# Performance work log

Measured on AMD Instinct MI355X. Metric: run time of the kernel, lower is better.

Reference implementation:

```python
import jax, jax.numpy as jnp
import numpy as np
import math

B, N, CS, CZ, H, C, P, PV, NB = 1, 512, 384, 128, 12, 16, 4, 8, 64


def quat_to_rot(q):
    q = q / jnp.clip(jnp.linalg.norm(q, axis=-1, keepdims=True), 1e-8)
    w, x, y, z = q[..., 0], q[..., 1], q[..., 2], q[..., 3]
    return jnp.stack([
        w*w + x*x - y*y - z*z, 2*(x*y - w*z), 2*(x*z + w*y),
        2*(x*y + w*z), w*w - x*x + y*y - z*z, 2*(y*z - w*x),
        2*(x*z - w*y), 2*(y*z + w*x), w*w - x*x - y*y + z*z,
    ], axis=-1).reshape(q.shape[:-1] + (3, 3))


def setup_inputs() -> dict:
    key = jax.random.key(0)
    ks = jax.random.split(key, 28)
    def n(k, shape, sc=1.0):
        return jax.random.normal(k, shape, jnp.float32) * sc
    s = n(ks[0], (B, N, CS))
    z = n(ks[1], (B, N, N, CZ))
    translations = n(ks[2], (B, N, 3)) * 4.0  # spread distances over 0-32A bins
    rotations = quat_to_rot(n(ks[3], (B, N, 4)))  # valid SO(3) frames
    mask = jnp.ones((B, N), dtype=bool)
    inv = lambda fan: 1.0 / math.sqrt(fan)
    return {
        's': s, 'z': z, 'translations': translations, 'rotations': rotations, 'mask': mask,
        'Wq': n(ks[4], (CS, H*C), inv(CS)), 'bq': n(ks[5], (H*C,), 0.01),
        'Wk': n(ks[6], (CS, H*C), inv(CS)), 'bk': n(ks[7], (H*C,), 0.01),
        'Wv': n(ks[8], (CS, H*C), inv(CS)), 'bv': n(ks[9], (H*C,), 0.01),
        'Wqp': n(ks[10], (CS, H*P*3), inv(CS)), 'bqp': n(ks[11], (H*P*3,), 0.01),
        'Wkp': n(ks[12], (CS, H*P*3), inv(CS)), 'bkp': n(ks[13], (H*P*3,), 0.01),
        'Wvp': n(ks[14], (CS, H*PV*3), inv(CS)), 'bvp': n(ks[15], (H*PV*3,), 0.01),
        'Wb': n(ks[16], (CZ, H), inv(CZ)), 'bb': n(ks[17], (H,), 0.01),
        'dist_emb': n(ks[18], (NB, H), 0.02),
        'scale_logits': n(ks[19], (3, H), 0.1),
        'head_weights': jnp.abs(n(ks[20], (H,))) * 0.2 + 0.8,
        'Wout': n(ks[21], (H*(C + PV*4 + CZ), CS), inv(H*(C + PV*4 + CZ))),
        'bout': n(ks[22], (CS,), 0.01),
    }


def reference(s, z, translations, rotations, mask, Wq, bq, Wk, bk, Wv, bv,
              Wqp, bqp, Wkp, bkp, Wvp, bvp, Wb, bb, dist_emb, scale_logits,
              head_weights, Wout, bout):
    b, n, _ = s.shape
    q = (s @ Wq + bq).reshape(b, n, H, C)
    k = (s @ Wk + bk).reshape(b, n, H, C)
    v = (s @ Wv + bv).reshape(b, n, H, C)
    q_pts = (s @ Wqp + bqp).reshape(b, n, H, P, 3)
    k_pts = (s @ Wkp + bkp).reshape(b, n, H, P, 3)
    v_pts = (s @ Wvp + bvp).reshape(b, n, H, PV, 3)
    t = translations[:, :, None, None, :]
    q_g = jnp.einsum('bnij,bnhpj->bnhpi', rotations, q_pts) + t
    k_g = jnp.einsum('bnij,bnhpj->bnhpi', rotations, k_pts) + t
    v_g = jnp.einsum('bnij,bnhpj->bnhpi', rotations, v_pts) + t
    scalar_logits = jnp.einsum('bnhc,bmhc->bnmh', q, k) / math.sqrt(C)
    # squared point distances, summed over points p and coords i, via expansion
    q_sq = (q_g**2).sum((-1, -2))  # (b, n, h)
    k_sq = (k_g**2).sum((-1, -2))
    cross = jnp.einsum('bnhpi,bmhpi->bnmh', q_g, k_g)
    point_dist = q_sq[:, :, None, :] + k_sq[:, None, :, :] - 2.0 * cross
    point_logits = -0.5 * point_dist * head_weights
    pair_bias = z @ Wb + bb  # (b, n, m, h)
    pair_dist = jnp.linalg.norm(
        translations[:, :, None, :] - translations[:, None, :, :], axis=-1)
    edges = jnp.linspace(0.0, 32.0, NB + 1)
    bins = jnp.clip(jnp.searchsorted(edges, pair_dist, side='left') - 1, 0, NB - 1)
    dist_bias = dist_emb[bins]
    local = (pair_dist <= 5.0).astype(s.dtype)
    medium = ((pair_dist > 5.0) & (pair_dist <= 15.0)).astype(s.dtype)
    scales = jnp.stack([local, medium, jnp.ones_like(pair_dist)], axis=-1)
    per_head = jax.nn.softmax(scale_logits, axis=0)  # (3, h)
    multiscale = jnp.einsum('bnms,sh->bnmh', scales, per_head)
    logits = scalar_logits + point_logits + pair_bias + dist_bias + multiscale
    m2d = mask[:, :, None] & mask[:, None, :]
    logits = jnp.where(m2d[..., None], logits, -10000.0)
    attn = jax.nn.softmax(logits.astype(jnp.float32), axis=2).astype(s.dtype)
    out_scalar = jnp.einsum('bnmh,bmhc->bnhc', attn, v)
    out_pts_g = jnp.einsum('bnmh,bmhpi->bnhpi', attn, v_g)
    out_pts_l = jnp.einsum('bnji,bnhpj->bnhpi', rotations, out_pts_g - t)  # R^T x
    out_norms = jnp.linalg.norm(out_pts_l, axis=-1)  # (b, n, h, pv)
    pair_feat = jnp.einsum('bnmh,bnmc->bnhc', attn, z)
    feats = jnp.concatenate(
        [out_scalar, out_pts_l.reshape(b, n, H, PV * 3), out_norms, pair_feat],
        axis=-1).reshape(b, n, -1)
    return feats @ Wout + bout
```

## Files before the change

### kernel.cpp

```cpp
#include <hip/hip_runtime.h>
#include <math.h>

#define N   512
#define CS  384
#define CZ  128
#define H   12
#define C   16
#define P   4
#define PV  8
#define NB  64
#define KSP 528
#define QKD 28
#define QPAD 68
#define APAD 516
#define ZPAD 132

#define OFF_Q    0
#define OFF_K    98304
#define OFF_V    196608
#define OFF_QP   294912
#define OFF_KP   368640
#define OFF_VP   442368
#define OFF_QG   589824
#define OFF_KG   663552
#define OFF_VG   737280
#define OFF_QSQ  884736
#define OFF_KSQ  890880
#define OFF_LOG  897024
#define OFF_FEAT 4042752

__global__ __launch_bounds__(256) void k_proj(
    const float* __restrict__ s,
    const float* __restrict__ Wq,  const float* __restrict__ bq,
    const float* __restrict__ Wk,  const float* __restrict__ bk,
    const float* __restrict__ Wv,  const float* __restrict__ bv,
    const float* __restrict__ Wqp, const float* __restrict__ bqp,
    const float* __restrict__ Wkp, const float* __restrict__ bkp,
    const float* __restrict__ Wvp, const float* __restrict__ bvp,
    float* __restrict__ ws)
{
    __shared__ float s_s[16*388];
    __shared__ float part[4*16*68];
    const int tid = threadIdx.x;
    const int n0  = blockIdx.y * 16;
    const int cq  = tid & 15;
    const int rg  = (tid >> 4) & 3;
    const int ks  = tid >> 6;
    const int gc  = blockIdx.x * 64 + cq * 4;
    for (int i = tid; i < 16*384; i += 256) {
        int r = i / 384, c = i - r*384;
        s_s[r*388 + c] = s[(n0 + r)*384 + c];
    }
    __syncthreads();
    const float* W; int width; int lc;
    if      (gc < 192) { W=Wq;  width=192; lc=gc;     }
    else if (gc < 384) { W=Wk;  width=192; lc=gc-192; }
    else if (gc < 576) { W=Wv;  width=192; lc=gc-384; }
    else if (gc < 720) { W=Wqp; width=144; lc=gc-576; }
    else if (gc < 864) { W=Wkp; width=144; lc=gc-720; }
    else               { W=Wvp; width=288; lc=gc-864; }
    float acc[4][4] = {{0.f}};
    const float* wp   = W + lc + (size_t)(ks*96)*width;
    const float* srow = s_s + (rg*4)*388 + ks*96;
    #pragma unroll 4
    for (int kk = 0; kk < 96; kk++) {
        float4 w4 = *(const float4*)(wp + (size_t)kk*width);
        #pragma unroll
        for (int r = 0; r < 4; r++) {
            float sv = srow[r*388 + kk];
            acc[r][0] += sv*w4.x; acc[r][1] += sv*w4.y;
            acc[r][2] += sv*w4.z; acc[r][3] += sv*w4.w;
        }
    }
    #pragma unroll
    for (int r = 0; r < 4; r++)
        *(float4*)(part + (ks*16 + rg*4 + r)*68 + cq*4) =
            make_float4(acc[r][0], acc[r][1], acc[r][2], acc[r][3]);
    __syncthreads();
    {
        const int row = tid >> 4;
        float4 sum = *(const float4*)(part + (0*16 + row)*68 + cq*4);
        #pragma unroll
        for (int k2 = 1; k2 < 4; k2++) {
            float4 p = *(const float4*)(part + (k2*16 + row)*68 + cq*4);
            sum.x += p.x; sum.y += p.y; sum.z += p.z; sum.w += p.w;
        }
        const float* b; float* dst; int w2, lc2;
        if      (gc < 192) { b=bq;  w2=192; lc2=gc;     dst=ws+OFF_Q;  }
        else if (gc < 384) { b=bk;  w2=192; lc2=gc-192; dst=ws+OFF_K;  }
        else if (gc < 576) { b=bv;  w2=192; lc2=gc-384; dst=ws+OFF_V;  }
        else if (gc < 720) { b=bqp; w2=144; lc2=gc-576; dst=ws+OFF_QP; }
        else if (gc < 864) { b=bkp; w2=144; lc2=gc-720; dst=ws+OFF_KP; }
        else               { b=bvp; w2=288; lc2=gc-864; dst=ws+OFF_VP; }
        float4 b4 = *(const float4*)(b + lc2);
        sum.x += b4.x; sum.y += b4.y; sum.z += b4.z; sum.w += b4.w;
        *(float4*)(dst + (size_t)(n0+row)*w2 + lc2) = sum;
    }
}

__global__ __launch_bounds__(192) void k_frames(
    const float* __restrict__ rot, const float* __restrict__ trans,
    float* __restrict__ ws)
{
    int n = blockIdx.x, tid = threadIdx.x;
    __shared__ float R[9], T[3], qg_s[144], kg_s[144];
    if (tid < 9) R[tid] = rot[n*9 + tid];
    if (tid < 3) T[tid] = trans[n*3 + tid];
    __syncthreads();
    if (tid < 48) {
        const float* lp = ws + OFF_QP + n*144 + tid*3;
        float l0=lp[0], l1=lp[1], l2=lp[2];
        float* gp = ws + OFF_QG + n*144 + tid*3;
        for (int i=0;i<3;i++){ float g = R[i*3+0]*l0 + R[i*3+1]*l1 + R[i*3+2]*l2 + T[i]; gp[i]=g; qg_s[tid*3+i]=g; }
    } else if (tid < 96) {
        int u = tid-48;
        const float* lp = ws + OFF_KP + n*144 + u*3;
        float l0=lp[0], l1=lp[1], l2=lp[2];
        float* gp = ws + OFF_KG + n*144 + u*3;
        for (int i=0;i<3;i++){ float g = R[i*3+0]*l0 + R[i*3+1]*l1 + R[i*3+2]*l2 + T[i]; gp[i]=g; kg_s[u*3+i]=g; }
    } else {
        int u = tid-96;
        const float* lp = ws + OFF_VP + n*288 + u*3;
        float l0=lp[0], l1=lp[1], l2=lp[2];
        float* gp = ws + OFF_VG + n*288 + u*3;
        for (int i=0;i<3;i++){ float g = R[i*3+0]*l0 + R[i*3+1]*l1 + R[i*3+2]*l2 + T[i]; gp[i]=g; }
    }
    __syncthreads();
    if (tid < 12) {
        float a=0;
        for (int d=0; d<12; d++){ float x=qg_s[tid*12+d]; a+=x*x; }
        ws[OFF_QSQ + n*12 + tid]=a;
    } else if (tid < 24) {
        int h = tid-12; float a=0;
        for (int d=0; d<12; d++){ float x=kg_s[h*12+d]; a+=x*x; }
        ws[OFF_KSQ + n*12 + h]=a;
    }
}

__global__ __launch_bounds__(256) void k_qkpt(
    const float* __restrict__ head_weights, float* __restrict__ ws)
{
    __shared__ float qs[QKD*QPAD], ks[QKD*QPAD], qa[64], kb[64];
    const int tid = threadIdx.x;
    const int m0 = blockIdx.x * 64, n0 = blockIdx.y * 64, h = blockIdx.z;
    const float hw = head_weights[h];
    for (int idx = tid; idx < 64*16; idx += 256) {
        int r = idx >> 4, c = idx & 15;
        qs[c*QPAD + r] = ws[OFF_Q + (n0+r)*192 + h*16 + c] * 0.25f;
        ks[c*QPAD + r] = ws[OFF_K + (m0+r)*192 + h*16 + c];
    }
    for (int idx = tid; idx < 64*12; idx += 256) {
        int r = idx / 12, c = idx % 12;
        qs[(16+c)*QPAD + r] = ws[OFF_QG + (n0+r)*144 + h*12 + c] * hw;
        ks[(16+c)*QPAD + r] = ws[OFF_KG + (m0+r)*144 + h*12 + c];
    }
    for (int idx = tid; idx < 64; idx += 256) {
        qa[idx] = -0.5f * hw * ws[OFF_QSQ + (n0+idx)*12 + h];
        kb[idx] = -0.5f * hw * ws[OFF_KSQ + (m0+idx)*12 + h];
    }
    __syncthreads();
    const int tx = tid & 15, ty = tid >> 4;
    float acc[4][4] = {{0.f}};
    #pragma unroll 4
    for (int d = 0; d < QKD; d++) {
        float4 a = *(const float4*)(qs + d*QPAD + ty*4);
        float4 b = *(const float4*)(ks + d*QPAD + tx*4);
        const float* ap = &a.x; const float* bp = &b.x;
        #pragma unroll
        for (int i=0;i<4;i++)
            #pragma unroll
            for (int j=0;j<4;j++) acc[i][j] += ap[i]*bp[j];
    }
    #pragma unroll
    for (int i=0;i<4;i++) {
        float ai = qa[ty*4+i];
        float4 r;
        r.x = acc[i][0] + ai + kb[tx*4+0];
        r.y = acc[i][1] + ai + kb[tx*4+1];
        r.z = acc[i][2] + ai + kb[tx*4+2];
        r.w = acc[i][3] + ai + kb[tx*4+3];
        *(float4*)(ws + OFF_LOG + ((size_t)(n0+ty*4+i)*H + h)*N + m0 + tx*4) = r;
    }
}

__global__ __launch_bounds__(256) void k_attn_all(
    const float* __restrict__ z, const float* __restrict__ trans,
    const float* __restrict__ rot,
    const float* __restrict__ Wb, const float* __restrict__ bb,
    const float* __restrict__ dist_emb, const float* __restrict__ scale_logits,
    float* __restrict__ ws)
{
    __shared__ float attn_s[H*APAD];
    __shared__ float zs[64*ZPAD];
    __shared__ float partial[4*64*13];
    __shared__ float Wb_s[CZ*12];
    __shared__ float og_s[288];
    __shared__ float sprob[36];
    float* part = zs;
    const int n = blockIdx.x, tid = threadIdx.x;
    const int lane = tid & 63, wave = tid >> 6;

    if (tid < 12) {
        float sa = scale_logits[tid], sb = scale_logits[12+tid], sc = scale_logits[24+tid];
        float mx = fmaxf(sa, fmaxf(sb, sc));
        float ea=__expf(sa-mx), eb=__expf(sb-mx), ec=__expf(sc-mx);
        float inv = 1.f/(ea+eb+ec);
        sprob[tid] = ea*inv; sprob[12+tid] = eb*inv; sprob[24+tid] = ec*inv;
    }
    for (int i = tid; i < 384; i += 256)
        *(float4*)(Wb_s + i*4) = *(const float4*)(Wb + i*4);

    const float4* asrc = (const float4*)(ws + OFF_LOG + (size_t)n*H*N);
    for (int i = tid; i < H*(N/4); i += 256) {
        int h = i >> 7, q = i & 127;
        *(float4*)(attn_s + h*APAD + q*4) = asrc[h*128 + q];
    }
    __syncthreads();

    {
        const float tnx = trans[n*3+0], tny = trans[n*3+1], tnz = trans[n*3+2];
        const int h0 = wave*3;
        const float bbv0 = bb[h0], bbv1 = bb[h0+1], bbv2 = bb[h0+2];
        const float spc0 = sprob[24+h0], spc1 = sprob[24+h0+1], spc2 = sprob[24+h0+2];
        const float spa0 = sprob[h0],    spa1 = sprob[h0+1],    spa2 = sprob[h0+2];
        const float spb0 = sprob[12+h0], spb1 = sprob[12+h0+1], spb2 = sprob[12+h0+2];
        const float4* zsrc4 = (const float4*)(z + (size_t)n*N*CZ);
        for (int chunk = 0; chunk < 8; chunk++) {
            #pragma unroll
            for (int pass = 0; pass < 8; pass++) {
                int idx = pass*256 + tid;
                float4 v = zsrc4[chunk*2048 + idx];
                *(float4*)(zs + (idx>>5)*ZPAD + (idx&31)*4) = v;
            }
            __syncthreads();
            {
                const float* zrow = zs + lane*ZPAD + wave*32;
                float a[12];
                #pragma unroll
                for (int h=0;h<12;h++) a[h]=0.f;
                #pragma unroll
                for (int c4=0;c4<8;c4++) {
                    float4 zq = *(const float4*)(zrow + c4*4);
                    const float* wr = Wb_s + (wave*32 + c4*4)*12;
                    const float* zp = &zq.x;
                    #pragma unroll
                    for (int j=0;j<4;j++) {
                        float4 w0 = *(const float4*)(wr + j*12);
                        float4 w1 = *(const float4*)(wr + j*12 + 4);
                        float4 w2 = *(const float4*)(wr + j*12 + 8);
                        float zj = zp[j];
                        a[0]+=zj*w0.x; a[1]+=zj*w0.y; a[2]+=zj*w0.z; a[3]+=zj*w0.w;
                        a[4]+=zj*w1.x; a[5]+=zj*w1.y; a[6]+=zj*w1.z; a[7]+=zj*w1.w;
                        a[8]+=zj*w2.x; a[9]+=zj*w2.y; a[10]+=zj*w2.z; a[11]+=zj*w2.w;
                    }
                }
                float* pdst = partial + (wave*64 + lane)*13;
                #pragma unroll
                for (int h=0;h<12;h++) pdst[h] = a[h];
            }
            __syncthreads();
            {
                const int m = chunk*64 + lane;
                float dx = tnx - trans[m*3+0];
                float dy = tny - trans[m*3+1];
                float dz = tnz - trans[m*3+2];
                float pdist = sqrtf(dx*dx+dy*dy+dz*dz);
                int bin = (int)ceilf(2.f*pdist) - 1;
                bin = bin < 0 ? 0 : (bin > NB-1 ? NB-1 : bin);
                const int ssel = (pdist <= 5.f) ? 0 : (pdist <= 15.f ? 1 : -1);
                float v0 = partial[(0*64+lane)*13 + h0]   + partial[(1*64+lane)*13 + h0]
                         + partial[(2*64+lane)*13 + h0]   + partial[(3*64+lane)*13 + h0];
                float v1 = partial[(0*64+lane)*13 + h0+1] + partial[(1*64+lane)*13 + h0+1]
                         + partial[(2*64+lane)*13 + h0+1] + partial[(3*64+lane)*13 + h0+1];
                float v2 = partial[(0*64+lane)*13 + h0+2] + partial[(1*64+lane)*13 + h0+2]
                         + partial[(2*64+lane)*13 + h0+2] + partial[(3*64+lane)*13 + h0+2];
                v0 += bbv0 + dist_emb[bin*12 + h0]   + spc0;
                v1 += bbv1 + dist_emb[bin*12 + h0+1] + spc1;
                v2 += bbv2 + dist_emb[bin*12 + h0+2] + spc2;
                if (ssel == 0)      { v0 += spa0; v1 += spa1; v2 += spa2; }
                else if (ssel == 1) { v0 += spb0; v1 += spb1; v2 += spb2; }
                attn_s[(h0  )*APAD + m] += v0;
                attn_s[(h0+1)*APAD + m] += v1;
                attn_s[(h0+2)*APAD + m] += v2;
            }
            __syncthreads();
        }
    }

    for (int h = wave; h < H; h += 4) {
        float* row = attn_s + h*APAD;
        float v[8]; float mx = -1e30f;
        #pragma unroll
        for (int j=0;j<8;j++){ v[j]=row[lane + j*64]; mx = fmaxf(mx, v[j]); }
        #pragma unroll
        for (int off=32; off>0; off>>=1) mx = fmaxf(mx, __shfl_xor(mx, off, 64));
        float sum = 0.f;
        #pragma unroll
        for (int j=0;j<8;j++){ v[j]=__expf(v[j]-mx); sum += v[j]; }
        #pragma unroll
        for (int off=32; off>0; off>>=1) sum += __shfl_xor(sum, off, 64);
        float inv = 1.f/sum;
        #pragma unroll
        for (int j=0;j<8;j++) row[lane + j*64] = v[j]*inv;
    }
    __syncthreads();

    const int cq = tid & 15;
    const int ms = tid >> 4;
    for (int ch = 0; ch < 2; ch++) {
        const float* zb = z + (size_t)n*N*CZ + ch*64 + cq*4;
        float4 acc[12];
        #pragma unroll
        for (int h=0; h<12; h++) acc[h] = make_float4(0.f,0.f,0.f,0.f);
        const int r0 = ms*32;
        #pragma unroll 2
        for (int rq = 0; rq < 8; rq++) {
            const int r = r0 + rq*4;
            float4 z0 = *(const float4*)(zb + (size_t)(r+0)*CZ);
            float4 z1 = *(const float4*)(zb + (size_t)(r+1)*CZ);
            float4 z2 = *(const float4*)(zb + (size_t)(r+2)*CZ);
            float4 z3 = *(const float4*)(zb + (size_t)(r+3)*CZ);
            #pragma unroll
            for (int h=0; h<12; h++) {
                float4 a4 = *(const float4*)(attn_s + h*APAD + r);
                acc[h].x += a4.x*z0.x + a4.y*z1.x + a4.z*z2.x + a4.w*z3.x;
                acc[h].y += a4.x*z0.y + a4.y*z1.y + a4.z*z2.y + a4.w*z3.y;
                acc[h].z += a4.x*z0.z + a4.y*z1.z + a4.z*z2.z + a4.w*z3.z;
                acc[h].w += a4.x*z0.w + a4.y*z1.w + a4.z*z2.w + a4.w*z3.w;
            }
        }
        #pragma unroll
        for (int h=0; h<12; h++) {
            acc[h].x += __shfl_xor(acc[h].x, 16, 64); acc[h].y += __shfl_xor(acc[h].y, 16, 64);
            acc[h].z += __shfl_xor(acc[h].z, 16, 64); acc[h].w += __shfl_xor(acc[h].w, 16, 64);
            acc[h].x += __shfl_xor(acc[h].x, 32, 64); acc[h].y += __shfl_xor(acc[h].y, 32, 64);
            acc[h].z += __shfl_xor(acc[h].z, 32, 64); acc[h].w += __shfl_xor(acc[h].w, 32, 64);
        }
        if (lane < 16) {
            #pragma unroll
            for (int h=0; h<12; h++)
                *(float4*)(part + (wave*12 + h)*64 + lane*4) = acc[h];
        }
        __syncthreads();
        if (tid < 192) {
            const int h = tid >> 4, c4 = tid & 15;
            float4 s4 = *(const float4*)(part + (0*12 + h)*64 + c4*4);
            #pragma unroll
            for (int w=1; w<4; w++) {
                float4 p = *(const float4*)(part + (w*12 + h)*64 + c4*4);
                s4.x += p.x; s4.y += p.y; s4.z += p.z; s4.w += p.w;
            }
            *(float4*)(ws + OFF_FEAT + (size_t)n*2112 + h*176 + 48 + ch*64 + c4*4) = s4;
        }
        __syncthreads();
    }

    if (tid < 240) {
        const int col4 = (tid % 120) * 4;
        const int msA  = tid / 120;
        const float* aptr; int astride, ah;
        if (col4 < 192) { ah = col4 >> 4;        aptr = ws + OFF_V  + col4;       astride = 192; }
        else            { ah = (col4-192) / 24;  aptr = ws + OFF_VG + (col4-192); astride = 288; }
        const float4* arow = (const float4*)(attn_s + ah*APAD);
        float4 acc = {0.f,0.f,0.f,0.f};
        #pragma unroll 2
        for (int mq = msA*64; mq < msA*64 + 64; mq++) {
            float4 a4 = arow[mq];
            const float* vp = aptr + (size_t)mq*4*astride;
            float4 v0 = *(const float4*)(vp);
            float4 v1 = *(const float4*)(vp + astride);
            float4 v2 = *(const float4*)(vp + 2*astride);
            float4 v3 = *(const float4*)(vp + 3*astride);
            acc.x += a4.x*v0.x + a4.y*v1.x + a4.z*v2.x + a4.w*v3.x;
            acc.y += a4.x*v0.y + a4.y*v1.y + a4.z*v2.y + a4.w*v3.y;
            acc.z += a4.x*v0.z + a4.y*v1.z + a4.z*v2.z + a4.w*v3.z;
            acc.w += a4.x*v0.w + a4.y*v1.w + a4.z*v2.w + a4.w*v3.w;
        }
        *(float4*)(part + tid*4) = acc;
    }
    __syncthreads();
    if (tid < 120) {
        const int col4 = tid * 4;
        float4 a = *(const float4*)(part + tid*4);
        float4 b = *(const float4*)(part + (tid+120)*4);
        a.x += b.x; a.y += b.y; a.z += b.z; a.w += b.w;
        if (col4 < 192) {
            const int ah = col4 >> 4;
            *(float4*)(ws + OFF_FEAT + (size_t)n*2112 + ah*176 + (col4 & 15)) = a;
        } else {
            *(float4*)(og_s + (col4 - 192)) = a;
        }
    }
    __syncthreads();
    if (tid < 96) {
        const int h = tid >> 3, p = tid & 7;
        float g0 = og_s[h*24 + p*3 + 0] - trans[n*3+0];
        float g1 = og_s[h*24 + p*3 + 1] - trans[n*3+1];
        float g2 = og_s[h*24 + p*3 + 2] - trans[n*3+2];
        const float* R = rot + n*9;
        float* fdst = ws + OFF_FEAT + (size_t)n*2112 + h*176;
        float nsq = 0.f;
        #pragma unroll
        for (int i=0;i<3;i++){
            float l = R[0*3+i]*g0 + R[1*3+i]*g1 + R[2*3+i]*g2;
            fdst[16 + p*3 + i] = l;
            nsq += l*l;
        }
        fdst[40 + p] = sqrtf(nsq);
    }
}

__global__ __launch_bounds__(384) void k_bias(
    const float* __restrict__ bout, float* __restrict__ out)
{
    out[(size_t)blockIdx.x*CS + threadIdx.x] = bout[threadIdx.x];
}

__global__ __launch_bounds__(256) void k_out(
    const float* __restrict__ Wout, const float* __restrict__ ws,
    float* __restrict__ out)
{
    __shared__ float f_s[16*KSP];
    __shared__ float part[4*16*68];
    const int tid = threadIdx.x;
    const int n0  = blockIdx.y * 16;
    const int k0  = blockIdx.z * KSP;
    const int cq  = tid & 15;
    const int rg  = (tid >> 4) & 3;
    const int ks  = tid >> 6;
    const int col = blockIdx.x * 64 + cq * 4;
    for (int i = tid; i < 16*KSP; i += 256) {
        int r = i / KSP, c = i - r*KSP;
        f_s[i] = ws[OFF_FEAT + (size_t)(n0 + r)*2112 + k0 + c];
    }
    __syncthreads();
    float acc[4][4] = {{0.f}};
    const float* wp = Wout + (size_t)(k0 + ks*132)*CS + col;
    const float* f0 = f_s + (rg*4)*KSP + ks*132;
    #pragma unroll 4
    for (int kk = 0; kk < 132; kk++) {
        float4 w4 = *(const float4*)(wp + (size_t)kk*CS);
        #pragma unroll
        for (int r = 0; r < 4; r++) {
            float fv = f0[r*KSP + kk];
            acc[r][0] += fv*w4.x; acc[r][1] += fv*w4.y;
            acc[r][2] += fv*w4.z; acc[r][3] += fv*w4.w;
        }
    }
    #pragma unroll
    for (int r = 0; r < 4; r++)
        *(float4*)(part + (ks*16 + rg*4 + r)*68 + cq*4) =
            make_float4(acc[r][0], acc[r][1], acc[r][2], acc[r][3]);
    __syncthreads();
    {
        const int row = tid >> 4;
        float4 s = *(const float4*)(part + (0*16 + row)*68 + cq*4);
        #pragma unroll
        for (int k2 = 1; k2 < 4; k2++) {
            float4 p = *(const float4*)(part + (k2*16 + row)*68 + cq*4);
            s.x += p.x; s.y += p.y; s.z += p.z; s.w += p.w;
        }
        float* o = out + (size_t)(n0+row)*CS + col;
        atomicAdd(o+0, s.x); atomicAdd(o+1, s.y);
        atomicAdd(o+2, s.z); atomicAdd(o+3, s.w);
    }
}

extern "C" void kernel_launch(void* const* d_in, const int* in_sizes, int n_in,
                              void* d_out, int out_size, void* d_ws, size_t ws_size,
                              hipStream_t stream) {
    const float* s     = (const float*)d_in[0];
    const float* z     = (const float*)d_in[1];
    const float* trans = (const float*)d_in[2];
    const float* rot   = (const float*)d_in[3];
    const float* Wq  = (const float*)d_in[5];  const float* bq  = (const float*)d_in[6];
    const float* Wk  = (const float*)d_in[7];  const float* bk  = (const float*)d_in[8];
    const float* Wv  = (const float*)d_in[9];  const float* bv  = (const float*)d_in[10];
    const float* Wqp = (const float*)d_in[11]; const float* bqp = (const float*)d_in[12];
    const float* Wkp = (const float*)d_in[13]; const float* bkp = (const float*)d_in[14];
    const float* Wvp = (const float*)d_in[15]; const float* bvp = (const float*)d_in[16];
    const float* Wb  = (const float*)d_in[17]; const float* bb  = (const float*)d_in[18];
    const float* dist_emb     = (const float*)d_in[19];
    const float* scale_logits = (const float*)d_in[20];
    const float* head_weights = (const float*)d_in[21];
    const float* Wout = (const float*)d_in[22]; const float* bout = (const float*)d_in[23];
    float* out = (float*)d_out;
    float* ws  = (float*)d_ws;

    k_proj<<<dim3(18, 32), 256, 0, stream>>>(s, Wq,bq, Wk,bk, Wv,bv, Wqp,bqp, Wkp,bkp, Wvp,bvp, ws);
    k_frames<<<N, 192, 0, stream>>>(rot, trans, ws);
    k_qkpt<<<dim3(8, 8, 12), 256, 0, stream>>>(head_weights, ws);
    k_attn_all<<<N, 256, 0, stream>>>(z, trans, rot, Wb, bb, dist_emb, scale_logits, ws);
    k_bias<<<N, CS, 0, stream>>>(bout, out);
    k_out<<<dim3(6, 32, 4), 256, 0, stream>>>(Wout, ws, out);
}
```

Baseline: 364.9 us.

## Split fused attention kernel into z-bias, softmax, and role-split matmul kernels

Breaks the monolithic per-row attention kernel into three launches. A z-bias kernel spreads each row's pair-bias work over four blocks and adds it to the logits in global memory. A separate softmax kernel normalises the logits in place. The aggregation kernel then runs two blocks per row: one computes the attention-weighted z features, the other the scalar and point value aggregation plus the frame transform. This raises the number of blocks and cuts per-block LDS use to improve occupancy. In exchange, the logits make extra round trips through global memory and there are two more kernel launches.

```diff
diff --git a/kernel.cpp b/kernel.cpp
--- a/kernel.cpp
+++ b/kernel.cpp
@@ -13,7 +13,7 @@
 #define QKD 28
 #define QPAD 68
 #define APAD 516
-#define ZPAD 132
+#define ZP2 132
 
 #define OFF_Q    0
 #define OFF_K    98304
@@ -183,22 +183,18 @@
     }
 }
 
-__global__ __launch_bounds__(256) void k_attn_all(
+__global__ __launch_bounds__(256) void k_zbias2(
     const float* __restrict__ z, const float* __restrict__ trans,
-    const float* __restrict__ rot,
     const float* __restrict__ Wb, const float* __restrict__ bb,
     const float* __restrict__ dist_emb, const float* __restrict__ scale_logits,
     float* __restrict__ ws)
 {
-    __shared__ float attn_s[H*APAD];
-    __shared__ float zs[64*ZPAD];
+    __shared__ float zs[64*ZP2];
     __shared__ float partial[4*64*13];
     __shared__ float Wb_s[CZ*12];
-    __shared__ float og_s[288];
     __shared__ float sprob[36];
-    float* part = zs;
-    const int n = blockIdx.x, tid = threadIdx.x;
-    const int lane = tid & 63, wave = tid >> 6;
+    const int mb = blockIdx.x, n = blockIdx.y;
+    const int tid = threadIdx.x, lane = tid & 63, wave = tid >> 6;
 
     if (tid < 12) {
         float sa = scale_logits[tid], sb = scale_logits[12+tid], sc = scale_logits[24+tid];
@@ -209,6 +205,110 @@
     }
     for (int i = tid; i < 384; i += 256)
         *(float4*)(Wb_s + i*4) = *(const float4*)(Wb + i*4);
+    __syncthreads();
+
+    const float tnx = trans[n*3+0], tny = trans[n*3+1], tnz = trans[n*3+2];
+    const int h0 = wave*3;
+
+    for (int chunk = 0; chunk < 2; chunk++) {
+        const int m0 = mb*128 + chunk*64;
+        const float4* zsrc4 = (const float4*)(z + ((size_t)n*N + m0)*CZ);
+        #pragma unroll
+        for (int p = 0; p < 8; p++) {
+            int idx = p*256 + tid;
+            float4 v = zsrc4[idx];
+            *(float4*)(zs + (idx>>5)*ZP2 + (idx&31)*4) = v;
+        }
+        __syncthreads();
+        {
+            const float* zrow = zs + lane*ZP2 + wave*32;
+            float a[12];
+            #pragma unroll
+            for (int h=0;h<12;h++) a[h]=0.f;
+            #pragma unroll
+            for (int c4=0;c4<8;c4++) {
+                float4 zq = *(const float4*)(zrow + c4*4);
+                const float* wr = Wb_s + (wave*32 + c4*4)*12;
+                const float* zp = &zq.x;
+                #pragma unroll
+                for (int j=0;j<4;j++) {
+                    float4 w0 = *(const float4*)(wr + j*12);
+                    float4 w1 = *(const float4*)(wr + j*12 + 4);
+                    float4 w2 = *(const float4*)(wr + j*12 + 8);
+                    float zj = zp[j];
+                    a[0]+=zj*w0.x; a[1]+=zj*w0.y; a[2]+=zj*w0.z; a[3]+=zj*w0.w;
+                    a[4]+=zj*w1.x; a[5]+=zj*w1.y; a[6]+=zj*w1.z; a[7]+=zj*w1.w;
+                    a[8]+=zj*w2.x; a[9]+=zj*w2.y; a[10]+=zj*w2.z; a[11]+=zj*w2.w;
+                }
+            }
+            float* pdst = partial + (wave*64 + lane)*13;
+            #pragma unroll
+            for (int h=0;h<12;h++) pdst[h] = a[h];
+        }
+        __syncthreads();
+        {
+            const int m = m0 + lane;
+            float dx = tnx - trans[m*3+0];
+            float dy = tny - trans[m*3+1];
+            float dz = tnz - trans[m*3+2];
+            float pdist = sqrtf(dx*dx+dy*dy+dz*dz);
+            int bin = (int)ceilf(2.f*pdist) - 1;
+            bin = bin < 0 ? 0 : (bin > NB-1 ? NB-1 : bin);
+            const int ssel = (pdist <= 5.f) ? 0 : (pdist <= 15.f ? 1 : -1);
+            float v0 = partial[(0*64+lane)*13 + h0]   + partial[(1*64+lane)*13 + h0]
+                     + partial[(2*64+lane)*13 + h0]   + partial[(3*64+lane)*13 + h0];
+            float v1 = partial[(0*64+lane)*13 + h0+1] + partial[(1*64+lane)*13 + h0+1]
+                     + partial[(2*64+lane)*13 + h0+1] + partial[(3*64+lane)*13 + h0+1];
+            float v2 = partial[(0*64+lane)*13 + h0+2] + partial[(1*64+lane)*13 + h0+2]
+                     + partial[(2*64+lane)*13 + h0+2] + partial[(3*64+lane)*13 + h0+2];
+            v0 += bb[h0]   + dist_emb[bin*12 + h0]   + sprob[24+h0];
+            v1 += bb[h0+1] + dist_emb[bin*12 + h0+1] + sprob[24+h0+1];
+            v2 += bb[h0+2] + dist_emb[bin*12 + h0+2] + sprob[24+h0+2];
+            if (ssel == 0)      { v0 += sprob[h0];    v1 += sprob[h0+1];    v2 += sprob[h0+2]; }
+            else if (ssel == 1) { v0 += sprob[12+h0]; v1 += sprob[12+h0+1]; v2 += sprob[12+h0+2]; }
+            float* lp = ws + OFF_LOG + ((size_t)n*H + h0)*N + m;
+            lp[0]   += v0;
+            lp[N]   += v1;
+            lp[2*N] += v2;
+        }
+        __syncthreads();
+    }
+}
+
+__global__ __launch_bounds__(256) void k_sm(float* __restrict__ ws)
+{
+    const int n = blockIdx.x, tid = threadIdx.x;
+    const int lane = tid & 63, wave = tid >> 6;
+    for (int h = wave; h < H; h += 4) {
+        float* row = ws + OFF_LOG + ((size_t)n*H + h)*N;
+        float4 a = *(const float4*)(row + lane*8);
+        float4 b = *(const float4*)(row + lane*8 + 4);
+        float mx = fmaxf(fmaxf(fmaxf(a.x,a.y),fmaxf(a.z,a.w)),
+                         fmaxf(fmaxf(b.x,b.y),fmaxf(b.z,b.w)));
+        #pragma unroll
+        for (int off=32; off>0; off>>=1) mx = fmaxf(mx, __shfl_xor(mx, off, 64));
+        a.x=__expf(a.x-mx); a.y=__expf(a.y-mx); a.z=__expf(a.z-mx); a.w=__expf(a.w-mx);
+        b.x=__expf(b.x-mx); b.y=__expf(b.y-mx); b.z=__expf(b.z-mx); b.w=__expf(b.w-mx);
+        float sum = a.x+a.y+a.z+a.w+b.x+b.y+b.z+b.w;
+        #pragma unroll
+        for (int off=32; off>0; off>>=1) sum += __shfl_xor(sum, off, 64);
+        float inv = 1.f/sum;
+        a.x*=inv; a.y*=inv; a.z*=inv; a.w*=inv;
+        b.x*=inv; b.y*=inv; b.z*=inv; b.w*=inv;
+        *(float4*)(row + lane*8)     = a;
+        *(float4*)(row + lane*8 + 4) = b;
+    }
+}
+
+__global__ __launch_bounds__(256) void k_attnmm(
+    const float* __restrict__ z, const float* __restrict__ trans,
+    const float* __restrict__ rot, float* __restrict__ ws)
+{
+    __shared__ float attn_s[H*APAD];
+    __shared__ float part[4*12*64];
+    __shared__ float og_s[288];
+    const int n = blockIdx.x, role = blockIdx.y, tid = threadIdx.x;
+    const int lane = tid & 63, wave = tid >> 6;
 
     const float4* asrc = (const float4*)(ws + OFF_LOG + (size_t)n*H*N);
     for (int i = tid; i < H*(N/4); i += 256) {
@@ -217,196 +317,110 @@
     }
     __syncthreads();
 
-    {
-        const float tnx = trans[n*3+0], tny = trans[n*3+1], tnz = trans[n*3+2];
-        const int h0 = wave*3;
-        const float bbv0 = bb[h0], bbv1 = bb[h0+1], bbv2 = bb[h0+2];
-        const float spc0 = sprob[24+h0], spc1 = sprob[24+h0+1], spc2 = sprob[24+h0+2];
-        const float spa0 = sprob[h0],    spa1 = sprob[h0+1],    spa2 = sprob[h0+2];
-        const float spb0 = sprob[12+h0], spb1 = sprob[12+h0+1], spb2 = sprob[12+h0+2];
-        const float4* zsrc4 = (const float4*)(z + (size_t)n*N*CZ);
-        for (int chunk = 0; chunk < 8; chunk++) {
-            #pragma unroll
-            for (int pass = 0; pass < 8; pass++) {
-                int idx = pass*256 + tid;
-                float4 v = zsrc4[chunk*2048 + idx];
-                *(float4*)(zs + (idx>>5)*ZPAD + (idx&31)*4) = v;
+    if (role == 0) {
+        const int cq = tid & 15;
+        const int ms = tid >> 4;
+        for (int ch = 0; ch < 2; ch++) {
+            const float* zb = z + (size_t)n*N*CZ + ch*64 + cq*4;
+            float4 acc[12];
+            #pragma unroll
+            for (int h=0; h<12; h++) acc[h] = make_float4(0.f,0.f,0.f,0.f);
+            const int r0 = ms*32;
+            #pragma unroll 2
+            for (int rq = 0; rq < 8; rq++) {
+                const int r = r0 + rq*4;
+                float4 z0 = *(const float4*)(zb + (size_t)(r+0)*CZ);
+                float4 z1 = *(const float4*)(zb + (size_t)(r+1)*CZ);
+                float4 z2 = *(const float4*)(zb + (size_t)(r+2)*CZ);
+                float4 z3 = *(const float4*)(zb + (size_t)(r+3)*CZ);
+                #pragma unroll
+                for (int h=0; h<12; h++) {
+                    float4 a4 = *(const float4*)(attn_s + h*APAD + r);
+                    acc[h].x += a4.x*z0.x + a4.y*z1.x + a4.z*z2.x + a4.w*z3.x;
+                    acc[h].y += a4.x*z0.y + a4.y*z1.y + a4.z*z2.y + a4.w*z3.y;
+                    acc[h].z += a4.x*z0.z + a4.y*z1.z + a4.z*z2.z + a4.w*z3.z;
+                    acc[h].w += a4.x*z0.w + a4.y*z1.w + a4.z*z2.w + a4.w*z3.w;
+                }
+            }
+            #pragma unroll
+            for (int h=0; h<12; h++) {
+                acc[h].x += __shfl_xor(acc[h].x, 16, 64); acc[h].y += __shfl_xor(acc[h].y, 16, 64);
+                acc[h].z += __shfl_xor(acc[h].z, 16, 64); acc[h].w += __shfl_xor(acc[h].w, 16, 64);
+                acc[h].x += __shfl_xor(acc[h].x, 32, 64); acc[h].y += __shfl_xor(acc[h].y, 32, 64);
+                acc[h].z += __shfl_xor(acc[h].z, 32, 64); acc[h].w += __shfl_xor(acc[h].w, 32, 64);
+            }
+            if (lane < 16) {
+                #pragma unroll
+                for (int h=0; h<12; h++)
+                    *(float4*)(part + (wave*12 + h)*64 + lane*4) = acc[h];
             }
             __syncthreads();
-            {
-                const float* zrow = zs + lane*ZPAD + wave*32;
-                float a[12];
+            if (tid < 192) {
+                const int h = tid >> 4, c4 = tid & 15;
+                float4 s4 = *(const float4*)(part + (0*12 + h)*64 + c4*4);
                 #pragma unroll
-                for (int h=0;h<12;h++) a[h]=0.f;
-                #pragma unroll
-                for (int c4=0;c4<8;c4++) {
-                    float4 zq = *(const float4*)(zrow + c4*4);
-                    const float* wr = Wb_s + (wave*32 + c4*4)*12;
-                    const float* zp = &zq.x;
-                    #pragma unroll
-                    for (int j=0;j<4;j++) {
-                        float4 w0 = *(const float4*)(wr + j*12);
-                        float4 w1 = *(const float4*)(wr + j*12 + 4);
-                        float4 w2 = *(const float4*)(wr + j*12 + 8);
-                        float zj = zp[j];
-                        a[0]+=zj*w0.x; a[1]+=zj*w0.y; a[2]+=zj*w0.z; a[3]+=zj*w0.w;
-                        a[4]+=zj*w1.x; a[5]+=zj*w1.y; a[6]+=zj*w1.z; a[7]+=zj*w1.w;
-                        a[8]+=zj*w2.x; a[9]+=zj*w2.y; a[10]+=zj*w2.z; a[11]+=zj*w2.w;
-                    }
+                for (int w=1; w<4; w++) {
+                    float4 p = *(const float4*)(part + (w*12 + h)*64 + c4*4);
+                    s4.x += p.x; s4.y += p.y; s4.z += p.z; s4.w += p.w;
                 }
-                float* pdst = partial + (wave*64 + lane)*13;
-                #pragma unroll
-                for (int h=0;h<12;h++) pdst[h] = a[h];
+                *(float4*)(ws + OFF_FEAT + (size_t)n*2112 + h*176 + 48 + ch*64 + c4*4) = s4;
             }
             __syncthreads();
-            {
-                const int m = chunk*64 + lane;
-                float dx = tnx - trans[m*3+0];
-                float dy = tny - trans[m*3+1];
-                float dz = tnz - trans[m*3+2];
-                float pdist = sqrtf(dx*dx+dy*dy+dz*dz);
-                int bin = (int)ceilf(2.f*pdist) - 1;
-                bin = bin < 0 ? 0 : (bin > NB-1 ? NB-1 : bin);
-                const int ssel = (pdist <= 5.f) ? 0 : (pdist <= 15.f ? 1 : -1);
-                float v0 = partial[(0*64+lane)*13 + h0]   + partial[(1*64+lane)*13 + h0]
-                         + partial[(2*64+lane)*13 + h0]   + partial[(3*64+lane)*13 + h0];
-                float v1 = partial[(0*64+lane)*13 + h0+1] + partial[(1*64+lane)*13 + h0+1]
-                         + partial[(2*64+lane)*13 + h0+1] + partial[(3*64+lane)*13 + h0+1];
-                float v2 = partial[(0*64+lane)*13 + h0+2] + partial[(1*64+lane)*13 + h0+2]
-                         + partial[(2*64+lane)*13 + h0+2] + partial[(3*64+lane)*13 + h0+2];
-                v0 += bbv0 + dist_emb[bin*12 + h0]   + spc0;
-                v1 += bbv1 + dist_emb[bin*12 + h0+1] + spc1;
-                v2 += bbv2 + dist_emb[bin*12 + h0+2] + spc2;
-                if (ssel == 0)      { v0 += spa0; v1 += spa1; v2 += spa2; }
-                else if (ssel == 1) { v0 += spb0; v1 += spb1; v2 += spb2; }
-                attn_s[(h0  )*APAD + m] += v0;
-                attn_s[(h0+1)*APAD + m] += v1;
-                attn_s[(h0+2)*APAD + m] += v2;
-            }
-            __syncthreads();
-        }
-    }
-
-    for (int h = wave; h < H; h += 4) {
-        float* row = attn_s + h*APAD;
-        float v[8]; float mx = -1e30f;
-        #pragma unroll
-        for (int j=0;j<8;j++){ v[j]=row[lane + j*64]; mx = fmaxf(mx, v[j]); }
-        #pragma unroll
-        for (int off=32; off>0; off>>=1) mx = fmaxf(mx, __shfl_xor(mx, off, 64));
-        float sum = 0.f;
-        #pragma unroll
-        for (int j=0;j<8;j++){ v[j]=__expf(v[j]-mx); sum += v[j]; }
-        #pragma unroll
-        for (int off=32; off>0; off>>=1) sum += __shfl_xor(sum, off, 64);
-        float inv = 1.f/sum;
-        #pragma unroll
-        for (int j=0;j<8;j++) row[lane + j*64] = v[j]*inv;
-    }
-    __syncthreads();
-
-    const int cq = tid & 15;
-    const int ms = tid >> 4;
-    for (int ch = 0; ch < 2; ch++) {
-        const float* zb = z + (size_t)n*N*CZ + ch*64 + cq*4;
-        float4 acc[12];
-        #pragma unroll
-        for (int h=0; h<12; h++) acc[h] = make_float4(0.f,0.f,0.f,0.f);
-        const int r0 = ms*32;
-        #pragma unroll 2
-        for (int rq = 0; rq < 8; rq++) {
-            const int r = r0 + rq*4;
-            float4 z0 = *(const float4*)(zb + (size_t)(r+0)*CZ);
-            float4 z1 = *(const float4*)(zb + (size_t)(r+1)*CZ);
-            float4 z2 = *(const float4*)(zb + (size_t)(r+2)*CZ);
-            float4 z3 = *(const float4*)(zb + (size_t)(r+3)*CZ);
-            #pragma unroll
-            for (int h=0; h<12; h++) {
-                float4 a4 = *(const float4*)(attn_s + h*APAD + r);
-                acc[h].x += a4.x*z0.x + a4.y*z1.x + a4.z*z2.x + a4.w*z3.x;
-                acc[h].y += a4.x*z0.y + a4.y*z1.y + a4.z*z2.y + a4.w*z3.y;
-                acc[h].z += a4.x*z0.z + a4.y*z1.z + a4.z*z2.z + a4.w*z3.z;
-                acc[h].w += a4.x*z0.w + a4.y*z1.w + a4.z*z2.w + a4.w*z3.w;
-            }
-        }
-        #pragma unroll
-        for (int h=0; h<12; h++) {
-            acc[h].x += __shfl_xor(acc[h].x, 16, 64); acc[h].y += __shfl_xor(acc[h].y, 16, 64);
-            acc[h].z += __shfl_xor(acc[h].z, 16, 64); acc[h].w += __shfl_xor(acc[h].w, 16, 64);
-            acc[h].x += __shfl_xor(acc[h].x, 32, 64); acc[h].y += __shfl_xor(acc[h].y, 32, 64);
-            acc[h].z += __shfl_xor(acc[h].z, 32, 64); acc[h].w += __shfl_xor(acc[h].w, 32, 64);
-        }
-        if (lane < 16) {
-            #pragma unroll
-            for (int h=0; h<12; h++)
-                *(float4*)(part + (wave*12 + h)*64 + lane*4) = acc[h];
+        }
+    } else {
+        if (tid < 240) {
+            const int col4 = (tid % 120) * 4;
+            const int msA  = tid / 120;
+            const float* aptr; int astride, ah;
+            if (col4 < 192) { ah = col4 >> 4;        aptr = ws + OFF_V  + col4;       astride = 192; }
+            else            { ah = (col4-192) / 24;  aptr = ws + OFF_VG + (col4-192); astride = 288; }
+            const float4* arow = (const float4*)(attn_s + ah*APAD);
+            float4 acc = {0.f,0.f,0.f,0.f};
+            #pragma unroll 2
+            for (int mq = msA*64; mq < msA*64 + 64; mq++) {
+                float4 a4 = arow[mq];
+                const float* vp = aptr + (size_t)mq*4*astride;
+                float4 v0 = *(const float4*)(vp);
+                float4 v1 = *(const float4*)(vp + astride);
+                float4 v2 = *(const float4*)(vp + 2*astride);
+                float4 v3 = *(const float4*)(vp + 3*astride);
+                acc.x += a4.x*v0.x + a4.y*v1.x + a4.z*v2.x + a4.w*v3.x;
+                acc.y += a4.x*v0.y + a4.y*v1.y + a4.z*v2.y + a4.w*v3.y;
+                acc.z += a4.x*v0.z + a4.y*v1.z + a4.z*v2.z + a4.w*v3.z;
+                acc.w += a4.x*v0.w + a4.y*v1.w + a4.z*v2.w + a4.w*v3.w;
+            }
+            *(float4*)(part + tid*4) = acc;
         }
         __syncthreads();
-        if (tid < 192) {
-            const int h = tid >> 4, c4 = tid & 15;
-            float4 s4 = *(const float4*)(part + (0*12 + h)*64 + c4*4);
-            #pragma unroll
-            for (int w=1; w<4; w++) {
-                float4 p = *(const float4*)(part + (w*12 + h)*64 + c4*4);
-                s4.x += p.x; s4.y += p.y; s4.z += p.z; s4.w += p.w;
-            }
-            *(float4*)(ws + OFF_FEAT + (size_t)n*2112 + h*176 + 48 + ch*64 + c4*4) = s4;
+        if (tid < 120) {
+            const int col4 = tid * 4;
+            float4 a = *(const float4*)(part + tid*4);
+            float4 b = *(const float4*)(part + (tid+120)*4);
+            a.x += b.x; a.y += b.y; a.z += b.z; a.w += b.w;
+            if (col4 < 192) {
+                const int ah = col4 >> 4;
+                *(float4*)(ws + OFF_FEAT + (size_t)n*2112 + ah*176 + (col4 & 15)) = a;
+            } else {
+                *(float4*)(og_s + (col4 - 192)) = a;
+            }
         }
         __syncthreads();
-    }
-
-    if (tid < 240) {
-        const int col4 = (tid % 120) * 4;
-        const int msA  = tid / 120;
-        const float* aptr; int astride, ah;
-        if (col4 < 192) { ah = col4 >> 4;        aptr = ws + OFF_V  + col4;       astride = 192; }
-        else            { ah = (col4-192) / 24;  aptr = ws + OFF_VG + (col4-192); astride = 288; }
-        const float4* arow = (const float4*)(attn_s + ah*APAD);
-        float4 acc = {0.f,0.f,0.f,0.f};
-        #pragma unroll 2
-        for (int mq = msA*64; mq < msA*64 + 64; mq++) {
-            float4 a4 = arow[mq];
-            const float* vp = aptr + (size_t)mq*4*astride;
-            float4 v0 = *(const float4*)(vp);
-            float4 v1 = *(const float4*)(vp + astride);
-            float4 v2 = *(const float4*)(vp + 2*astride);
-            float4 v3 = *(const float4*)(vp + 3*astride);
-            acc.x += a4.x*v0.x + a4.y*v1.x + a4.z*v2.x + a4.w*v3.x;
-            acc.y += a4.x*v0.y + a4.y*v1.y + a4.z*v2.y + a4.w*v3.y;
-            acc.z += a4.x*v0.z + a4.y*v1.z + a4.z*v2.z + a4.w*v3.z;
-            acc.w += a4.x*v0.w + a4.y*v1.w + a4.z*v2.w + a4.w*v3.w;
-        }
-        *(float4*)(part + tid*4) = acc;
-    }
-    __syncthreads();
-    if (tid < 120) {
-        const int col4 = tid * 4;
-        float4 a = *(const float4*)(part + tid*4);
-        float4 b = *(const float4*)(part + (tid+120)*4);
-        a.x += b.x; a.y += b.y; a.z += b.z; a.w += b.w;
-        if (col4 < 192) {
-            const int ah = col4 >> 4;
-            *(float4*)(ws + OFF_FEAT + (size_t)n*2112 + ah*176 + (col4 & 15)) = a;
-        } else {
-            *(float4*)(og_s + (col4 - 192)) = a;
-        }
-    }
-    __syncthreads();
-    if (tid < 96) {
-        const int h = tid >> 3, p = tid & 7;
-        float g0 = og_s[h*24 + p*3 + 0] - trans[n*3+0];
-        float g1 = og_s[h*24 + p*3 + 1] - trans[n*3+1];
-        float g2 = og_s[h*24 + p*3 + 2] - trans[n*3+2];
-        const float* R = rot + n*9;
-        float* fdst = ws + OFF_FEAT + (size_t)n*2112 + h*176;
-        float nsq = 0.f;
-        #pragma unroll
-        for (int i=0;i<3;i++){
-            float l = R[0*3+i]*g0 + R[1*3+i]*g1 + R[2*3+i]*g2;
-            fdst[16 + p*3 + i] = l;
-            nsq += l*l;
-        }
-        fdst[40 + p] = sqrtf(nsq);
+        if (tid < 96) {
+            const int h = tid >> 3, p = tid & 7;
+            float g0 = og_s[h*24 + p*3 + 0] - trans[n*3+0];
+            float g1 = og_s[h*24 + p*3 + 1] - trans[n*3+1];
+            float g2 = og_s[h*24 + p*3 + 2] - trans[n*3+2];
+            const float* R = rot + n*9;
+            float* fdst = ws + OFF_FEAT + (size_t)n*2112 + h*176;
+            float nsq = 0.f;
+            #pragma unroll
+            for (int i=0;i<3;i++){
+                float l = R[0*3+i]*g0 + R[1*3+i]*g1 + R[2*3+i]*g2;
+                fdst[16 + p*3 + i] = l;
+                nsq += l*l;
+            }
+            fdst[40 + p] = sqrtf(nsq);
+        }
     }
 }
 
@@ -490,7 +504,9 @@
     k_proj<<<dim3(18, 32), 256, 0, stream>>>(s, Wq,bq, Wk,bk, Wv,bv, Wqp,bqp, Wkp,bkp, Wvp,bvp, ws);
     k_frames<<<N, 192, 0, stream>>>(rot, trans, ws);
     k_qkpt<<<dim3(8, 8, 12), 256, 0, stream>>>(head_weights, ws);
-    k_attn_all<<<N, 256, 0, stream>>>(z, trans, rot, Wb, bb, dist_emb, scale_logits, ws);
+    k_zbias2<<<dim3(4, N), 256, 0, stream>>>(z, trans, Wb, bb, dist_emb, scale_logits, ws);
+    k_sm<<<N, 256, 0, stream>>>(ws);
+    k_attnmm<<<dim3(N, 2), 256, 0, stream>>>(z, trans, rot, ws);
     k_bias<<<N, CS, 0, stream>>>(bout, out);
     k_out<<<dim3(6, 32, 4), 256, 0, stream>>>(Wout, ws, out);
 }
```

Result: faster. 343.8 us (-5.8%).
